# Kernel tuning notes

Hardware: AMD Instinct MI355X
Metric: run time of the kernel (lower is better)

## Reference

```python
import jax, jax.numpy as jnp
import numpy as np


def gru_cell(x, h, Wih, Whh, bih, bhh):
    # torch GRU cell, gate order r, z, n
    gi = x @ Wih.T + bih
    gh = h @ Whh.T + bhh
    ir, iz, inn = jnp.split(gi, 3, axis=-1)
    hr, hz, hn = jnp.split(gh, 3, axis=-1)
    r = jax.nn.sigmoid(ir + hr)
    z = jax.nn.sigmoid(iz + hz)
    n = jnp.tanh(inn + r * hn)
    return (1.0 - z) * n + z * h


def setup_inputs() -> dict:
    key = jax.random.key(0)
    ks = jax.random.split(key, 24)
    S, T, B, E, H, V = 64, 64, 32, 512, 1024, 32000
    sc_e = 1.0 / np.sqrt(E)
    sc_h = 1.0 / np.sqrt(H)

    def rn(i, shape, sc):
        return jax.random.normal(ks[i], shape, jnp.float32) * sc

    return {
        "src": jax.random.randint(ks[0], (S, B), 0, V),
        "trg": jax.random.randint(ks[1], (T, B), 0, V),
        "emb": rn(2, (V, E), 0.02),
        # encoder forward-direction GRU
        "Wih_f": rn(3, (3 * H, E), sc_e), "Whh_f": rn(4, (3 * H, H), sc_h),
        "bih_f": rn(5, (3 * H,), sc_h), "bhh_f": rn(6, (3 * H,), sc_h),
        # encoder backward-direction GRU
        "Wih_b": rn(7, (3 * H, E), sc_e), "Whh_b": rn(8, (3 * H, H), sc_h),
        "bih_b": rn(9, (3 * H,), sc_h), "bhh_b": rn(10, (3 * H,), sc_h),
        # attention: Linear(2H -> H) and scoring vector v
        "Wa": rn(11, (H, 2 * H), sc_h), "ba": rn(12, (H,), sc_h),
        "v": rn(13, (H,), sc_h),
        # decoder GRU: input is [embedded(E); context(H)]
        "Wih_d": rn(14, (3 * H, E + H), sc_h), "Whh_d": rn(15, (3 * H, H), sc_h),
        "bih_d": rn(16, (3 * H,), sc_h), "bhh_d": rn(17, (3 * H,), sc_h),
        # output head Linear(2H -> V)
        "Wout": rn(18, (V, 2 * H), sc_h), "bout": rn(19, (V,), sc_h),
    }


def reference(src, trg, emb, Wih_f, Whh_f, bih_f, bhh_f, Wih_b, Whh_b, bih_b, bhh_b,
              Wa, ba, v, Wih_d, Whh_d, bih_d, bhh_d, Wout, bout):
    S, B = src.shape
    H = Whh_f.shape[1]

    # ---- encoder: bidirectional GRU, fwd+bwd output halves summed ----
    src_emb = emb[src]  # [S, B, E]
    h0 = jnp.zeros((B, H), src_emb.dtype)

    def step_f(h, x):
        h2 = gru_cell(x, h, Wih_f, Whh_f, bih_f, bhh_f)
        return h2, h2

    def step_b(h, x):
        h2 = gru_cell(x, h, Wih_b, Whh_b, bih_b, bhh_b)
        return h2, h2

    h_fwd, out_f = jax.lax.scan(step_f, h0, src_emb)
    _, out_b_rev = jax.lax.scan(step_b, h0, src_emb[::-1])
    enc_out = out_f + out_b_rev[::-1]          # [S, B, H]
    enc_bt = enc_out.transpose(1, 0, 2)        # [B, S, H]

    # ---- decoder with teacher forcing (ratio fixed to 1.0) ----
    dec_tokens = jnp.concatenate([src[-1:], trg[:-1]], axis=0)  # [T, B]
    dec_emb = emb[dec_tokens]                                   # [T, B, E]

    def dec_step(h, e_t):
        # Bahdanau attention: relu(Linear([h; enc])) scored by v
        hrep = jnp.broadcast_to(h[:, None, :], enc_bt.shape)    # [B, S, H]
        energy = jax.nn.relu(jnp.concatenate([hrep, enc_bt], -1) @ Wa.T + ba)
        scores = energy @ v                                     # [B, S]
        a = jax.nn.softmax(scores, axis=1)
        ctx = jnp.einsum('bs,bsh->bh', a, enc_bt)               # [B, H]
        rnn_in = jnp.concatenate([e_t, ctx], axis=-1)           # [B, E+H]
        h_new = gru_cell(rnn_in, h, Wih_d, Whh_d, bih_d, bhh_d)
        logits = jnp.concatenate([h_new, ctx], -1) @ Wout.T + bout  # [B, V]
        return h_new, logits

    _, outputs = jax.lax.scan(dec_step, h_fwd, dec_emb)  # [T, B, V]
    return outputs
```

## Files before the change

kernel.cpp:

```cpp
#include <hip/hip_runtime.h>
#include <hip/hip_bf16.h>

#define S_ 64
#define T_ 64
#define B_ 32
#define E_ 512
#define H_ 1024
#define V_ 32000
#define H3 3072
#define H2 2048
#define EH 1536

typedef unsigned short u16;
typedef unsigned int u32;
typedef unsigned long long u64;
typedef __attribute__((ext_vector_type(8))) short bf16x8;
typedef __attribute__((ext_vector_type(4))) float f32x4;

#define MFMA3(ACC, AH_, AL_, BH_, BL_)                                              \
    ACC = __builtin_amdgcn_mfma_f32_16x16x32_bf16(AL_, BH_, ACC, 0, 0, 0);          \
    ACC = __builtin_amdgcn_mfma_f32_16x16x32_bf16(AH_, BL_, ACC, 0, 0, 0);          \
    ACC = __builtin_amdgcn_mfma_f32_16x16x32_bf16(AH_, BH_, ACC, 0, 0, 0);

__device__ __forceinline__ void splitf(float x, u16& h, u16& l) {
    u32 xb = __float_as_uint(x);
    u32 hb = (xb + 0x7FFFu + ((xb >> 16) & 1u)) & 0xFFFF0000u;
    h = (u16)(hb >> 16);
    float lf = x - __uint_as_float(hb);
    u32 lb = __float_as_uint(lf);
    l = (u16)((lb + 0x7FFFu + ((lb >> 16) & 1u)) >> 16);
}

__device__ __forceinline__ float bf2f(u16 v) { return __uint_as_float(((u32)v) << 16); }

__device__ __forceinline__ void load_lds16(const void* g, void* l) {
    __builtin_amdgcn_global_load_lds((const __attribute__((address_space(1))) u32*)g,
                                     (__attribute__((address_space(3))) u32*)l, 16, 0, 0);
}

__device__ __forceinline__ bf16x8 ld_sys16(const u16* p) {
    union { bf16x8 v; u64 q[2]; } u;
    const u64* q = (const u64*)p;
    u.q[0] = __hip_atomic_load(q,     __ATOMIC_RELAXED, __HIP_MEMORY_SCOPE_SYSTEM);
    u.q[1] = __hip_atomic_load(q + 1, __ATOMIC_RELAXED, __HIP_MEMORY_SCOPE_SYSTEM);
    return u.v;
}
__device__ __forceinline__ float ld_sysf(const float* p) {
    return __hip_atomic_load(p, __ATOMIC_RELAXED, __HIP_MEMORY_SCOPE_SYSTEM);
}
__device__ __forceinline__ void st_sysf(float* p, float v) {
    __hip_atomic_store(p, v, __ATOMIC_RELAXED, __HIP_MEMORY_SCOPE_SYSTEM);
}
__device__ __forceinline__ void st_sysu16(u16* p, u16 v) {
    __hip_atomic_store(p, v, __ATOMIC_RELAXED, __HIP_MEMORY_SCOPE_SYSTEM);
}

__device__ __forceinline__ void gbar(int* cnt, int* flag, int nblk, int blk, int& gen) {
    __syncthreads();
    if (threadIdx.x == 0) {
        gen += 1;
        asm volatile("s_waitcnt vmcnt(0)" ::: "memory");
        __hip_atomic_fetch_add(&cnt[(blk & 7) << 5], 1, __ATOMIC_RELAXED,
                               __HIP_MEMORY_SCOPE_SYSTEM);
        if (blk == 0) {
            const int target = nblk * gen;
            for (;;) {
                int sum = 0;
#pragma unroll
                for (int j = 0; j < 8; ++j)
                    sum += __hip_atomic_load(&cnt[j << 5], __ATOMIC_RELAXED,
                                             __HIP_MEMORY_SCOPE_SYSTEM);
                if (sum >= target) break;
                __builtin_amdgcn_s_sleep(2);
            }
#pragma unroll
            for (int j = 0; j < 8; ++j)
                __hip_atomic_store(&flag[j << 5], gen, __ATOMIC_RELAXED,
                                   __HIP_MEMORY_SCOPE_SYSTEM);
        } else {
            while (__hip_atomic_load(&flag[(blk & 7) << 5], __ATOMIC_RELAXED,
                                     __HIP_MEMORY_SCOPE_SYSTEM) < gen)
                __builtin_amdgcn_s_sleep(2);
        }
    }
    __syncthreads();
}

__global__ void k_embed_src_split(const int* __restrict__ src, const float* __restrict__ emb,
                                  u16* __restrict__ hi, u16* __restrict__ lo) {
    int row = blockIdx.x;
    int tok = src[row];
    int c = threadIdx.x * 4;
    float4 v = *reinterpret_cast<const float4*>(emb + (size_t)tok * E_ + c);
    ushort4 h, l;
    splitf(v.x, h.x, l.x); splitf(v.y, h.y, l.y);
    splitf(v.z, h.z, l.z); splitf(v.w, h.w, l.w);
    *reinterpret_cast<ushort4*>(hi + (size_t)row * E_ + c) = h;
    *reinterpret_cast<ushort4*>(lo + (size_t)row * E_ + c) = l;
}

__global__ void k_embed_dec_split(const int* __restrict__ src, const int* __restrict__ trg,
                                  const float* __restrict__ emb,
                                  u16* __restrict__ hi, u16* __restrict__ lo) {
    int row = blockIdx.x;
    int t = row >> 5, b = row & 31;
    int tok = (t == 0) ? src[(S_ - 1) * B_ + b] : trg[(t - 1) * B_ + b];
    int c = threadIdx.x * 4;
    float4 v = *reinterpret_cast<const float4*>(emb + (size_t)tok * E_ + c);
    ushort4 h, l;
    splitf(v.x, h.x, l.x); splitf(v.y, h.y, l.y);
    splitf(v.z, h.z, l.z); splitf(v.w, h.w, l.w);
    *reinterpret_cast<ushort4*>(hi + (size_t)row * E_ + c) = h;
    *reinterpret_cast<ushort4*>(lo + (size_t)row * E_ + c) = l;
}

__global__ __launch_bounds__(256) void k_split(const float* __restrict__ in, int ld, int cols4,
                                               u16* __restrict__ hi, u16* __restrict__ lo) {
    int c4 = blockIdx.x * 256 + threadIdx.x;
    if (c4 >= cols4) return;
    size_t r = blockIdx.y;
    float4 v = *reinterpret_cast<const float4*>(in + r * ld + (size_t)c4 * 4);
    ushort4 h, l;
    splitf(v.x, h.x, l.x); splitf(v.y, h.y, l.y);
    splitf(v.z, h.z, l.z); splitf(v.w, h.w, l.w);
    size_t o = (r * cols4 + c4) * 4;
    *reinterpret_cast<ushort4*>(hi + o) = h;
    *reinterpret_cast<ushort4*>(lo + o) = l;
}

__global__ __launch_bounds__(256) void k_split_sum_enc(
    const float* __restrict__ ef, const float* __restrict__ eb, float* __restrict__ es,
    u16* __restrict__ hi, u16* __restrict__ lo) {
    size_t r = blockIdx.y;
    int c4 = threadIdx.x * 4;
    float4 va = *reinterpret_cast<const float4*>(ef + r * H_ + c4);
    float4 vb = *reinterpret_cast<const float4*>(eb + r * H_ + c4);
    float4 v; v.x = va.x + vb.x; v.y = va.y + vb.y; v.z = va.z + vb.z; v.w = va.w + vb.w;
    *reinterpret_cast<float4*>(es + r * H_ + c4) = v;
    ushort4 h, l;
    splitf(v.x, h.x, l.x); splitf(v.y, h.y, l.y);
    splitf(v.z, h.z, l.z); splitf(v.w, h.w, l.w);
    *reinterpret_cast<ushort4*>(hi + r * H_ + c4) = h;
    *reinterpret_cast<ushort4*>(lo + r * H_ + c4) = l;
}

__global__ void k_wsplit_perm(const float* __restrict__ src, int ld, int coff,
                              u16* __restrict__ hi, u16* __restrict__ lo) {
    int r = blockIdx.x;
    int i = r / 3, g = r - i * 3;
    const float* p = src + (size_t)(g * H_ + i) * ld + coff;
    int c = threadIdx.x * 4;
    float4 v = *reinterpret_cast<const float4*>(p + c);
    ushort4 h, l;
    splitf(v.x, h.x, l.x); splitf(v.y, h.y, l.y);
    splitf(v.z, h.z, l.z); splitf(v.w, h.w, l.w);
    *reinterpret_cast<ushort4*>(hi + (size_t)r * H_ + c) = h;
    *reinterpret_cast<ushort4*>(lo + (size_t)r * H_ + c) = l;
}

__global__ __launch_bounds__(256, 2) void k_gemm_mfma3(
    const u16* __restrict__ Ah, const u16* __restrict__ Al,
    const u16* __restrict__ Bh, const u16* __restrict__ Bl,
    const float* __restrict__ bias, float* __restrict__ C,
    int ldc, int K)
{
    __shared__ u16 ls[4][128 * 32];
    const int tid = threadIdx.x;
    const int lane = tid & 63, w = tid >> 6;
    const int wr = w >> 1, wc = w & 1;
    const size_t m0 = (size_t)blockIdx.x * 128, n0 = (size_t)blockIdx.y * 128;

    const int c0 = (w * 2) * 64 + lane;
    const int r0 = c0 >> 2, kc0 = (c0 & 3) << 3;
    const size_t rstep = (size_t)16 * K;
    const u16* gAh = Ah + (m0 + r0) * K + kc0;
    const u16* gAl = Al + (m0 + r0) * K + kc0;
    const u16* gBh = Bh + (n0 + r0) * K + kc0;
    const u16* gBl = Bl + (n0 + r0) * K + kc0;
    const int lo0 = c0 * 8;

    const int frow = lane & 15, fk = (lane >> 4) << 3;
    const int offA = (wr * 64 + frow) * 32 + fk;
    const int offB = (wc * 64 + frow) * 32 + fk;

    f32x4 acc[4][4] = {};

    for (int k0 = 0; k0 < K; k0 += 32) {
        load_lds16(gAh + k0, &ls[0][lo0]);
        load_lds16(gAh + rstep + k0, &ls[0][lo0 + 512]);
        load_lds16(gAl + k0, &ls[1][lo0]);
        load_lds16(gAl + rstep + k0, &ls[1][lo0 + 512]);
        load_lds16(gBh + k0, &ls[2][lo0]);
        load_lds16(gBh + rstep + k0, &ls[2][lo0 + 512]);
        load_lds16(gBl + k0, &ls[3][lo0]);
        load_lds16(gBl + rstep + k0, &ls[3][lo0 + 512]);
        __syncthreads();

        bf16x8 fAh[4], fAl[4], fBh[4], fBl[4];
#pragma unroll
        for (int m = 0; m < 4; ++m) {
            fAh[m] = *reinterpret_cast<const bf16x8*>(&ls[0][offA + m * 512]);
            fAl[m] = *reinterpret_cast<const bf16x8*>(&ls[1][offA + m * 512]);
        }
#pragma unroll
        for (int n = 0; n < 4; ++n) {
            fBh[n] = *reinterpret_cast<const bf16x8*>(&ls[2][offB + n * 512]);
            fBl[n] = *reinterpret_cast<const bf16x8*>(&ls[3][offB + n * 512]);
        }
#pragma unroll
        for (int m = 0; m < 4; ++m)
#pragma unroll
            for (int n = 0; n < 4; ++n) {
                MFMA3(acc[m][n], fAh[m], fAl[m], fBh[n], fBl[n]);
            }
        __syncthreads();
    }

    const int crow0 = wr * 64 + ((lane >> 4) << 2);
    const int ccol0 = wc * 64 + (lane & 15);
#pragma unroll
    for (int n = 0; n < 4; ++n) {
        const size_t col = n0 + ccol0 + n * 16;
        const float bv = bias ? bias[col] : 0.f;
#pragma unroll
        for (int m = 0; m < 4; ++m)
#pragma unroll
            for (int r = 0; r < 4; ++r)
                C[(m0 + crow0 + m * 16 + r) * (size_t)ldc + col] = acc[m][n][r] + bv;
    }
}

__global__ __launch_bounds__(256) void k_enc_persist(
    const u16* __restrict__ whhf_h, const u16* __restrict__ whhf_l,
    const u16* __restrict__ whhb_h, const u16* __restrict__ whhb_l,
    const float* __restrict__ gi_f, const float* __restrict__ gi_b,
    const float* __restrict__ bhh_f, const float* __restrict__ bhh_b,
    u16* __restrict__ hfH0, u16* __restrict__ hfL0,
    u16* __restrict__ hfH1, u16* __restrict__ hfL1,
    u16* __restrict__ hbH0, u16* __restrict__ hbL0,
    u16* __restrict__ hbH1, u16* __restrict__ hbL1,
    float* __restrict__ enc_f, float* __restrict__ enc_b,
    int* __restrict__ cnt, int* __restrict__ flag)
{
    __shared__ __align__(16) char smem[107008];
    u16* lH = (u16*)smem;
    float* ex = (float*)(smem + 98304);
    float* hloc = (float*)(smem + 104704);

    const int blk = blockIdx.x, tid = threadIdx.x;
    const int lane = tid & 63, w = tid >> 6;
    const int dir = blk >> 6, c = blk & 63;
    const int i0 = c * 16;
    const size_t rowbase = (size_t)c * 48;
    const u16* WH = (dir ? whhb_h : whhf_h) + rowbase * 1024;
    const u16* WL = (dir ? whhb_l : whhf_l) + rowbase * 1024;
    const float* gi = dir ? gi_b : gi_f;
    const float* bhh = dir ? bhh_b : bhh_f;
    float* encd = dir ? enc_b : enc_f;
    int gen = 0;

    for (int ch = tid; ch < 6144; ch += 256) {
        int r = ch >> 7, kc = (ch & 127) << 3;
        *(bf16x8*)&lH[r * 1024 + (kc ^ ((r & 7) << 3))] =
            *(const bf16x8*)&WH[(size_t)r * 1024 + kc];
    }
    for (int q = tid; q < 512; q += 256) hloc[q] = 0.f;
    __syncthreads();

    const int frow = lane & 15, fk8 = (lane >> 4) << 3;
    const int cb = lane & 15, rb0 = (lane >> 4) << 2;

    for (int t = 0; t < 64; ++t) {
        const int a = t & 1;
        const u16* rH = dir ? (a ? hbH1 : hbH0) : (a ? hfH1 : hfH0);
        const u16* rL = dir ? (a ? hbL1 : hbL0) : (a ? hfL1 : hfL0);
        u16* oH = dir ? (a ? hbH0 : hbH1) : (a ? hfH0 : hfH1);
        u16* oL = dir ? (a ? hbL0 : hbL1) : (a ? hfL0 : hfL1);
        const int s = dir ? 63 - t : t;

        if (w < 2) {
            f32x4 acc0 = {}, acc1 = {};
            const int lrB = w * 16 + frow;
            const int bsw = (lrB & 7) << 3;
            const u16* gBl = WL + (size_t)lrB * 1024;
#pragma unroll 4
            for (int k0 = 0; k0 < 1024; k0 += 32) {
                int kc = k0 + fk8;
                bf16x8 bH = *(const bf16x8*)&lH[lrB * 1024 + (kc ^ bsw)];
                bf16x8 bL = *(const bf16x8*)&gBl[kc];
                bf16x8 aH0 = ld_sys16(&rH[frow * 1024 + kc]);
                bf16x8 aL0 = ld_sys16(&rL[frow * 1024 + kc]);
                bf16x8 aH1 = ld_sys16(&rH[(16 + frow) * 1024 + kc]);
                bf16x8 aL1 = ld_sys16(&rL[(16 + frow) * 1024 + kc]);
                MFMA3(acc0, aH0, aL0, bH, bL);
                MFMA3(acc1, aH1, aL1, bH, bL);
            }
            int pc = w * 16 + cb;
#pragma unroll
            for (int r = 0; r < 4; ++r) {
                ex[pc * 33 + rb0 + r] = acc0[r];
                ex[pc * 33 + 16 + rb0 + r] = acc1[r];
            }
        } else {
            f32x4 acc0 = {}, acc1 = {};
            const int m = w - 2;
            const int lrB = 32 + frow;
            const int bsw = (lrB & 7) << 3;
            const u16* gBl = WL + (size_t)lrB * 1024;
#pragma unroll 2
            for (int k0 = 0; k0 < 1024; k0 += 64) {
                {
                    int kc = k0 + fk8;
                    bf16x8 bH = *(const bf16x8*)&lH[lrB * 1024 + (kc ^ bsw)];
                    bf16x8 bL = *(const bf16x8*)&gBl[kc];
                    bf16x8 aH = ld_sys16(&rH[(m * 16 + frow) * 1024 + kc]);
                    bf16x8 aL = ld_sys16(&rL[(m * 16 + frow) * 1024 + kc]);
                    MFMA3(acc0, aH, aL, bH, bL);
                }
                {
                    int kc = k0 + 32 + fk8;
                    bf16x8 bH = *(const bf16x8*)&lH[lrB * 1024 + (kc ^ bsw)];
                    bf16x8 bL = *(const bf16x8*)&gBl[kc];
                    bf16x8 aH = ld_sys16(&rH[(m * 16 + frow) * 1024 + kc]);
                    bf16x8 aL = ld_sys16(&rL[(m * 16 + frow) * 1024 + kc]);
                    MFMA3(acc1, aH, aL, bH, bL);
                }
            }
            f32x4 accs = acc0 + acc1;
            int pc = 32 + cb;
#pragma unroll
            for (int r = 0; r < 4; ++r)
                ex[pc * 33 + m * 16 + rb0 + r] = accs[r];
        }
        __syncthreads();

        {
            const int il = tid & 15, bb = tid >> 4;
            const int i = i0 + il;
#pragma unroll
            for (int q = 0; q < 2; ++q) {
                int b = bb + q * 16;
                float ghr = ex[(3 * il + 0) * 33 + b] + bhh[i];
                float ghz = ex[(3 * il + 1) * 33 + b] + bhh[H_ + i];
                float ghn = ex[(3 * il + 2) * 33 + b] + bhh[2 * H_ + i];
                size_t gio = (size_t)(s * B_ + b) * H3 + i;
                float gir = gi[gio], giz = gi[gio + H_], gin = gi[gio + 2 * H_];
                float rr = 1.f / (1.f + expf(-(gir + ghr)));
                float zz = 1.f / (1.f + expf(-(giz + ghz)));
                float nn = tanhf(gin + rr * ghn);
                float hold = hloc[b * 16 + il];
                float hnew = (1.f - zz) * nn + zz * hold;
                hloc[b * 16 + il] = hnew;
                u16 hh, hl; splitf(hnew, hh, hl);
                st_sysu16(&oH[b * 1024 + i], hh);
                st_sysu16(&oL[b * 1024 + i], hl);
                encd[((size_t)b * 64 + s) * H_ + i] = hnew;
            }
        }
        gbar(cnt, flag, 128, blk, gen);
    }
}

__global__ __launch_bounds__(256) void k_dec_persist(
    const u16* __restrict__ wah, const u16* __restrict__ wal,
    const u16* __restrict__ wgh, const u16* __restrict__ wgl,
    const u16* __restrict__ wdh, const u16* __restrict__ wdl,
    const float* __restrict__ gi_e, const float* __restrict__ bhh_d,
    const float* __restrict__ ep, const float* __restrict__ vvec,
    const float* __restrict__ enc,
    u16* __restrict__ hH, u16* __restrict__ hL,
    float* __restrict__ hwa, float* __restrict__ scores,
    u16* __restrict__ ctxH, u16* __restrict__ ctxL,
    float* __restrict__ states, int* __restrict__ cnt, int* __restrict__ flag)
{
    __shared__ __align__(16) char smem[140288];
    u16* lWH  = (u16*)smem;
    u16* lWL  = (u16*)(smem + 32768);
    u16* lDH  = (u16*)(smem + 65536);
    float* lenc = (float*)(smem + 98304);
    float* ex1a = (float*)(smem + 131072);
    float* ex1b = (float*)(smem + 133120);
    float* ex2a = (float*)(smem + 135168);
    float* ex2b = (float*)(smem + 137216);
    float* aw   = (float*)(smem + 139264);
    float* hloc = (float*)(smem + 139520);

    const int bid = blockIdx.x, tid = threadIdx.x;
    const int lane = tid & 63, w = tid >> 6;
    const int frow = lane & 15, fk8 = (lane >> 4) << 3;
    const int b3 = bid >> 3, sl = bid & 7;
    int gen = 0;

    for (int ch = tid; ch < 2048; ch += 256) {
        int r = ch >> 7, kc = (ch & 127) << 3;
        int sw = kc ^ ((r & 7) << 3);
        const u16 *sH, *sL;
        if (r < 4) { sH = wah + ((size_t)bid * 4 + r) * 1024;
                     sL = wal + ((size_t)bid * 4 + r) * 1024; }
        else       { sH = wgh + ((size_t)bid * 12 + r - 4) * 1024;
                     sL = wgl + ((size_t)bid * 12 + r - 4) * 1024; }
        *(bf16x8*)&lWH[r * 1024 + sw] = *(const bf16x8*)&sH[kc];
        *(bf16x8*)&lWL[r * 1024 + sw] = *(const bf16x8*)&sL[kc];
    }
    for (int ch = tid; ch < 2048; ch += 256) {
        int r = ch >> 7, kc = (ch & 127) << 3;
        int sw = kc ^ ((r & 7) << 3);
        int rowg = (r < 12) ? bid * 12 + r : bid * 12;
        *(bf16x8*)&lDH[r * 1024 + sw] = *(const bf16x8*)&wdh[(size_t)rowg * 1024 + kc];
    }
    for (int ch = tid; ch < 2048; ch += 256) {
        int s = ch >> 5, c4 = (ch & 31) << 2;
        *(float4*)&lenc[s * 128 + c4] =
            *(const float4*)&enc[((size_t)b3 * 64 + s) * 1024 + sl * 128 + c4];
    }
    if (tid < 128) {
        int b = tid >> 2, u = bid * 4 + (tid & 3);
        hloc[tid] = bf2f(hH[b * 1024 + u]) + bf2f(hL[b * 1024 + u]);
    }
    float vreg[16];
#pragma unroll
    for (int i = 0; i < 16; ++i) vreg[i] = vvec[lane + i * 64];
    __syncthreads();

    const int mt = w & 1, kh = w >> 1;
    const int bsw = (frow & 7) << 3;
    const int rowg = (frow < 12) ? bid * 12 + frow : bid * 12;
    const u16* gDl = wdl + (size_t)rowg * 1024;
    const int exw = (mt * 16 + ((lane >> 4) << 2)) * 16 + frow;

    for (int t = 0; t < 64; ++t) {
        {
            float* exA = kh ? ex1b : ex1a;
            f32x4 acc = {};
            const int ar0 = (mt * 16 + frow) * 1024;
            const int ke = kh * 512 + 512;
#pragma unroll 4
            for (int k0 = kh * 512; k0 < ke; k0 += 32) {
                int kc = k0 + fk8;
                bf16x8 aH = ld_sys16(&hH[ar0 + kc]);
                bf16x8 aL = ld_sys16(&hL[ar0 + kc]);
                bf16x8 bH = *(const bf16x8*)&lWH[frow * 1024 + (kc ^ bsw)];
                bf16x8 bL = *(const bf16x8*)&lWL[frow * 1024 + (kc ^ bsw)];
                MFMA3(acc, aH, aL, bH, bL);
            }
#pragma unroll
            for (int r = 0; r < 4; ++r) exA[exw + r * 16] = acc[r];
        }
        __syncthreads();
        if (tid < 128) {
            int b = tid >> 2, col = tid & 3;
            st_sysf(&hwa[b * 1024 + bid * 4 + col],
                    ex1a[b * 16 + col] + ex1b[b * 16 + col]);
        }
        gbar(cnt, flag, 256, bid, gen);

#pragma unroll
        for (int q2 = 0; q2 < 2; ++q2) {
            int s = sl * 8 + w * 2 + q2;
            const float* epr = ep + ((size_t)b3 * 64 + s) * 1024;
            const float* hr = hwa + b3 * 1024;
            float a2 = 0.f;
#pragma unroll
            for (int i = 0; i < 16; ++i) {
                int j = lane + i * 64;
                a2 += fmaxf(ld_sysf(&hr[j]) + epr[j], 0.f) * vreg[i];
            }
            for (int off = 32; off; off >>= 1) a2 += __shfl_down(a2, off);
            if (lane == 0) st_sysf(&scores[b3 * 64 + s], a2);
        }
        gbar(cnt, flag, 256, bid, gen);

        if (tid < 64) {
            float sc = ld_sysf(&scores[b3 * 64 + tid]);
            float m = sc;
            for (int off = 32; off; off >>= 1) m = fmaxf(m, __shfl_xor(m, off));
            float e = expf(sc - m);
            float sum = e;
            for (int off = 32; off; off >>= 1) sum += __shfl_xor(sum, off);
            aw[tid] = e / sum;
        }
        __syncthreads();
        if (tid < 128) {
            int c = tid;
            float x = 0.f;
#pragma unroll 8
            for (int s = 0; s < 64; ++s) x += aw[s] * lenc[s * 128 + c];
            states[((size_t)t * 32 + b3) * 2048 + 1024 + sl * 128 + c] = x;
            u16 hh, hl; splitf(x, hh, hl);
            st_sysu16(&ctxH[b3 * 1024 + sl * 128 + c], hh);
            st_sysu16(&ctxL[b3 * 1024 + sl * 128 + c], hl);
        }
        gbar(cnt, flag, 256, bid, gen);

        {
            float* exD = kh ? ex2b : ex2a;
            f32x4 acc = {};
            const int ar0 = (mt * 16 + frow) * 1024;
            const int ke = kh * 512 + 512;
#pragma unroll 4
            for (int k0 = kh * 512; k0 < ke; k0 += 32) {
                int kc = k0 + fk8;
                bf16x8 aH = ld_sys16(&ctxH[ar0 + kc]);
                bf16x8 aL = ld_sys16(&ctxL[ar0 + kc]);
                bf16x8 bH = *(const bf16x8*)&lDH[frow * 1024 + (kc ^ bsw)];
                bf16x8 bL = *(const bf16x8*)&gDl[kc];
                MFMA3(acc, aH, aL, bH, bL);
            }
#pragma unroll
            for (int r = 0; r < 4; ++r) exD[exw + r * 16] = acc[r];
        }
        __syncthreads();
        if (tid < 128) {
            int b = tid >> 2, ui = tid & 3;
            int u = bid * 4 + ui;
            float gicr = ex2a[b * 16 + 3 * ui + 0] + ex2b[b * 16 + 3 * ui + 0];
            float gicz = ex2a[b * 16 + 3 * ui + 1] + ex2b[b * 16 + 3 * ui + 1];
            float gicn = ex2a[b * 16 + 3 * ui + 2] + ex2b[b * 16 + 3 * ui + 2];
            float ghr = ex1a[b * 16 + 4 + 3 * ui + 0] + ex1b[b * 16 + 4 + 3 * ui + 0] + bhh_d[u];
            float ghz = ex1a[b * 16 + 4 + 3 * ui + 1] + ex1b[b * 16 + 4 + 3 * ui + 1] + bhh_d[H_ + u];
            float ghn = ex1a[b * 16 + 4 + 3 * ui + 2] + ex1b[b * 16 + 4 + 3 * ui + 2] + bhh_d[2 * H_ + u];
            size_t ge = ((size_t)t * 32 + b) * 3072;
            float gir = gi_e[ge + u] + gicr;
            float giz = gi_e[ge + 1024 + u] + gicz;
            float gin = gi_e[ge + 2048 + u] + gicn;
            float rr = 1.f / (1.f + expf(-(gir + ghr)));
            float zz = 1.f / (1.f + expf(-(giz + ghz)));
            float nn = tanhf(gin + rr * ghn);
            float hold = hloc[tid];
            float hnew = (1.f - zz) * nn + zz * hold;
            hloc[tid] = hnew;
            u16 hh, hl; splitf(hnew, hh, hl);
            st_sysu16(&hH[b * 1024 + u], hh);
            st_sysu16(&hL[b * 1024 + u], hl);
            states[((size_t)t * 32 + b) * 2048 + u] = hnew;
        }
        gbar(cnt, flag, 256, bid, gen);
    }
}

extern "C" void kernel_launch(void* const* d_in, const int* in_sizes, int n_in,
                              void* d_out, int out_size, void* d_ws, size_t ws_size,
                              hipStream_t stream) {
    const int*   src   = (const int*)d_in[0];
    const int*   trg   = (const int*)d_in[1];
    const float* emb   = (const float*)d_in[2];
    const float* Wih_f = (const float*)d_in[3];
    const float* Whh_f = (const float*)d_in[4];
    const float* bih_f = (const float*)d_in[5];
    const float* bhh_f = (const float*)d_in[6];
    const float* Wih_b = (const float*)d_in[7];
    const float* Whh_b = (const float*)d_in[8];
    const float* bih_b = (const float*)d_in[9];
    const float* bhh_b = (const float*)d_in[10];
    const float* Wa    = (const float*)d_in[11];
    const float* ba    = (const float*)d_in[12];
    const float* vv    = (const float*)d_in[13];
    const float* Wih_d = (const float*)d_in[14];
    const float* Whh_d = (const float*)d_in[15];
    const float* bih_d = (const float*)d_in[16];
    const float* bhh_d = (const float*)d_in[17];
    const float* Wout  = (const float*)d_in[18];
    const float* bout  = (const float*)d_in[19];
    float* out = (float*)d_out;
    (void)in_sizes; (void)n_in; (void)out_size; (void)ws_size;

    float* w = (float*)d_ws;
    size_t o = 0;
    auto alloc = [&](size_t n) { float* p = w + o; o += n; return p; };
    float* gi_f  = alloc((size_t)S_ * B_ * H3);
    float* gi_b  = alloc((size_t)S_ * B_ * H3);
    float* enc_f = alloc((size_t)B_ * S_ * H_);
    float* enc_b = alloc((size_t)B_ * S_ * H_);
    float* enc   = alloc((size_t)B_ * S_ * H_);
    float* ep    = alloc((size_t)B_ * S_ * H_);
    float* hwa   = alloc((size_t)B_ * H_);
    float* scores = alloc(B_ * S_);
    float* barf  = alloc(1024);
    int* cntE  = (int*)barf;
    int* flagE = cntE + 256;
    int* cntD  = cntE + 512;
    int* flagD = cntE + 768;
    float* gi_e   = gi_f;
    float* states = gi_b;

    u16* wu = (u16*)(w + o);
    size_t ou = 0;
    auto alloc16 = [&](size_t n) { u16* p = wu + ou; ou += n; return p; };
    u16* semb_h  = alloc16((size_t)S_ * B_ * E_);  u16* semb_l  = alloc16((size_t)S_ * B_ * E_);
    u16* demb_h  = alloc16((size_t)T_ * B_ * E_);  u16* demb_l  = alloc16((size_t)T_ * B_ * E_);
    u16* wihf_h  = alloc16((size_t)H3 * E_);       u16* wihf_l  = alloc16((size_t)H3 * E_);
    u16* wihb_h  = alloc16((size_t)H3 * E_);       u16* wihb_l  = alloc16((size_t)H3 * E_);
    u16* wihd_h  = alloc16((size_t)H3 * E_);       u16* wihd_l  = alloc16((size_t)H3 * E_);
    u16* wae_h   = alloc16((size_t)H_ * H_);       u16* wae_l   = alloc16((size_t)H_ * H_);
    u16* enc_h   = alloc16((size_t)B_ * S_ * H_);  u16* enc_l   = alloc16((size_t)B_ * S_ * H_);
    u16* st_h    = alloc16((size_t)T_ * B_ * H2);  u16* st_l    = alloc16((size_t)T_ * B_ * H2);
    u16* wout_h  = alloc16((size_t)6400 * H2);     u16* wout_l  = alloc16((size_t)6400 * H2);
    u16* whhf_h  = alloc16((size_t)H3 * H_);       u16* whhf_l  = alloc16((size_t)H3 * H_);
    u16* whhb_h  = alloc16((size_t)H3 * H_);       u16* whhb_l  = alloc16((size_t)H3 * H_);
    u16* wgh     = alloc16((size_t)H3 * H_);       u16* wgl     = alloc16((size_t)H3 * H_);
    u16* wdh     = alloc16((size_t)H3 * H_);       u16* wdl     = alloc16((size_t)H3 * H_);
    u16* wah     = alloc16((size_t)H_ * H_);       u16* wal     = alloc16((size_t)H_ * H_);
    u16* hsf_h[2] = {alloc16(B_ * H_), alloc16(B_ * H_)};
    u16* hsf_l[2] = {alloc16(B_ * H_), alloc16(B_ * H_)};
    u16* hsb_h[2] = {alloc16(B_ * H_), alloc16(B_ * H_)};
    u16* hsb_l[2] = {alloc16(B_ * H_), alloc16(B_ * H_)};
    u16* ctx_h   = alloc16(B_ * H_);               u16* ctx_l   = alloc16(B_ * H_);

    hipMemsetAsync(barf, 0, 1024 * sizeof(float), stream);
    hipMemsetAsync(hsf_h[0], 0, B_ * H_ * sizeof(u16), stream);
    hipMemsetAsync(hsf_l[0], 0, B_ * H_ * sizeof(u16), stream);
    hipMemsetAsync(hsb_h[0], 0, B_ * H_ * sizeof(u16), stream);
    hipMemsetAsync(hsb_l[0], 0, B_ * H_ * sizeof(u16), stream);

    k_embed_src_split<<<S_ * B_, 128, 0, stream>>>(src, emb, semb_h, semb_l);
    k_embed_dec_split<<<T_ * B_, 128, 0, stream>>>(src, trg, emb, demb_h, demb_l);

    k_split<<<dim3(1, H3), 256, 0, stream>>>(Wih_f, E_, E_ / 4, wihf_h, wihf_l);
    k_split<<<dim3(1, H3), 256, 0, stream>>>(Wih_b, E_, E_ / 4, wihb_h, wihb_l);
    k_split<<<dim3(1, H3), 256, 0, stream>>>(Wih_d, EH, E_ / 4, wihd_h, wihd_l);
    k_split<<<dim3(1, H_), 256, 0, stream>>>(Wa + H_, H2, H_ / 4, wae_h, wae_l);
    k_split<<<dim3(1, H_), 256, 0, stream>>>(Wa, H2, H_ / 4, wah, wal);
    k_wsplit_perm<<<H3, 256, 0, stream>>>(Whh_f, H_, 0, whhf_h, whhf_l);
    k_wsplit_perm<<<H3, 256, 0, stream>>>(Whh_b, H_, 0, whhb_h, whhb_l);
    k_wsplit_perm<<<H3, 256, 0, stream>>>(Whh_d, H_, 0, wgh, wgl);
    k_wsplit_perm<<<H3, 256, 0, stream>>>(Wih_d, EH, E_, wdh, wdl);

    k_gemm_mfma3<<<dim3(16, 24), 256, 0, stream>>>(semb_h, semb_l, wihf_h, wihf_l,
                                                   bih_f, gi_f, H3, E_);
    k_gemm_mfma3<<<dim3(16, 24), 256, 0, stream>>>(semb_h, semb_l, wihb_h, wihb_l,
                                                   bih_b, gi_b, H3, E_);

    k_enc_persist<<<128, 256, 0, stream>>>(
        whhf_h, whhf_l, whhb_h, whhb_l, gi_f, gi_b, bhh_f, bhh_b,
        hsf_h[0], hsf_l[0], hsf_h[1], hsf_l[1],
        hsb_h[0], hsb_l[0], hsb_h[1], hsb_l[1],
        enc_f, enc_b, cntE, flagE);

    k_split_sum_enc<<<dim3(1, B_ * S_), 256, 0, stream>>>(enc_f, enc_b, enc, enc_h, enc_l);
    k_gemm_mfma3<<<dim3(16, 8), 256, 0, stream>>>(enc_h, enc_l, wae_h, wae_l,
                                                  ba, ep, H_, H_);
    k_gemm_mfma3<<<dim3(16, 24), 256, 0, stream>>>(demb_h, demb_l, wihd_h, wihd_l,
                                                   bih_d, gi_e, H3, E_);

    k_dec_persist<<<256, 256, 0, stream>>>(
        wah, wal, wgh, wgl, wdh, wdl, gi_e, bhh_d, ep, vv, enc,
        hsf_h[0], hsf_l[0], hwa, scores, ctx_h, ctx_l, states, cntD, flagD);

    k_split<<<dim3(2, T_ * B_), 256, 0, stream>>>(states, H2, H2 / 4, st_h, st_l);
    for (int p = 0; p < 5; ++p) {
        k_split<<<dim3(2, 6400), 256, 0, stream>>>(Wout + (size_t)p * 6400 * H2, H2,
                                                   H2 / 4, wout_h, wout_l);
        k_gemm_mfma3<<<dim3(16, 50), 256, 0, stream>>>(st_h, st_l, wout_h, wout_l,
                                                       bout + p * 6400,
                                                       out + (size_t)p * 6400, V_, H2);
    }
}
```

Measured before the change: 4.762 ms.

## Stage hidden state in LDS per step and split K across waves in encoder

The encoder persistent kernel no longer keeps the high half of its Whh slice resident in LDS. Each timestep it copies the shared hidden state (hi/lo bf16 halves) from global into swizzled LDS, so it is read from memory once per block instead of once per wave. The 2x3 output tiles are split along K into two halves, giving 12 balanced jobs (3 per wave), and the partial sums are reduced through two exchange buffers. Both weight halves are now streamed from global/L2 every step, and the larger LDS footprint plus an extra barrier per step add cost.

```diff
diff --git a/kernel.cpp b/kernel.cpp
--- a/kernel.cpp
+++ b/kernel.cpp
@@ -242,30 +242,25 @@
     float* __restrict__ enc_f, float* __restrict__ enc_b,
     int* __restrict__ cnt, int* __restrict__ flag)
 {
-    __shared__ __align__(16) char smem[107008];
-    u16* lH = (u16*)smem;
-    float* ex = (float*)(smem + 98304);
-    float* hloc = (float*)(smem + 104704);
+    __shared__ __align__(16) char smem[145792];
+    u16* lAh  = (u16*)smem;
+    u16* lAl  = (u16*)(smem + 65536);
+    float* ex0 = (float*)(smem + 131072);
+    float* ex1 = (float*)(smem + 137408);
+    float* hloc = (float*)(smem + 143744);
 
     const int blk = blockIdx.x, tid = threadIdx.x;
     const int lane = tid & 63, w = tid >> 6;
     const int dir = blk >> 6, c = blk & 63;
     const int i0 = c * 16;
-    const size_t rowbase = (size_t)c * 48;
-    const u16* WH = (dir ? whhb_h : whhf_h) + rowbase * 1024;
-    const u16* WL = (dir ? whhb_l : whhf_l) + rowbase * 1024;
+    const u16* WH = (dir ? whhb_h : whhf_h) + (size_t)c * 48 * 1024;
+    const u16* WL = (dir ? whhb_l : whhf_l) + (size_t)c * 48 * 1024;
     const float* gi = dir ? gi_b : gi_f;
     const float* bhh = dir ? bhh_b : bhh_f;
     float* encd = dir ? enc_b : enc_f;
     int gen = 0;
 
-    for (int ch = tid; ch < 6144; ch += 256) {
-        int r = ch >> 7, kc = (ch & 127) << 3;
-        *(bf16x8*)&lH[r * 1024 + (kc ^ ((r & 7) << 3))] =
-            *(const bf16x8*)&WH[(size_t)r * 1024 + kc];
-    }
     for (int q = tid; q < 512; q += 256) hloc[q] = 0.f;
-    __syncthreads();
 
     const int frow = lane & 15, fk8 = (lane >> 4) << 3;
     const int cb = lane & 15, rb0 = (lane >> 4) << 2;
@@ -278,59 +273,42 @@
         u16* oL = dir ? (a ? hbL0 : hbL1) : (a ? hfL0 : hfL1);
         const int s = dir ? 63 - t : t;
 
-        if (w < 2) {
-            f32x4 acc0 = {}, acc1 = {};
-            const int lrB = w * 16 + frow;
-            const int bsw = (lrB & 7) << 3;
-            const u16* gBl = WL + (size_t)lrB * 1024;
+#pragma unroll
+        for (int ch0 = 0; ch0 < 4096; ch0 += 256) {
+            int ch = ch0 + tid;
+            int r = ch >> 7, kc = (ch & 127) << 3;
+            int sw = kc ^ ((r & 7) << 3);
+            *(bf16x8*)&lAh[r * 1024 + sw] = ld_sys16(&rH[r * 1024 + kc]);
+            *(bf16x8*)&lAl[r * 1024 + sw] = ld_sys16(&rL[r * 1024 + kc]);
+        }
+        __syncthreads();
+
+#pragma unroll
+        for (int jj = 0; jj < 3; ++jj) {
+            const int j = w * 3 + jj;
+            const int m = j & 1;
+            const int n = (j >> 1) % 3;
+            const int kh = j / 6;
+            const int arow = m * 16 + frow;
+            const int asw = (arow & 7) << 3;
+            const u16* gBh = WH + (size_t)(n * 16 + frow) * 1024;
+            const u16* gBl = WL + (size_t)(n * 16 + frow) * 1024;
+            f32x4 acc = {};
+            const int ke = kh * 512 + 512;
 #pragma unroll 4
-            for (int k0 = 0; k0 < 1024; k0 += 32) {
+            for (int k0 = kh * 512; k0 < ke; k0 += 32) {
                 int kc = k0 + fk8;
-                bf16x8 bH = *(const bf16x8*)&lH[lrB * 1024 + (kc ^ bsw)];
+                bf16x8 aH = *(const bf16x8*)&lAh[arow * 1024 + (kc ^ asw)];
+                bf16x8 aL = *(const bf16x8*)&lAl[arow * 1024 + (kc ^ asw)];
+                bf16x8 bH = *(const bf16x8*)&gBh[kc];
                 bf16x8 bL = *(const bf16x8*)&gBl[kc];
-                bf16x8 aH0 = ld_sys16(&rH[frow * 1024 + kc]);
-                bf16x8 aL0 = ld_sys16(&rL[frow * 1024 + kc]);
-                bf16x8 aH1 = ld_sys16(&rH[(16 + frow) * 1024 + kc]);
-                bf16x8 aL1 = ld_sys16(&rL[(16 + frow) * 1024 + kc]);
-                MFMA3(acc0, aH0, aL0, bH, bL);
-                MFMA3(acc1, aH1, aL1, bH, bL);
+                MFMA3(acc, aH, aL, bH, bL);
             }
-            int pc = w * 16 + cb;
-#pragma unroll
-            for (int r = 0; r < 4; ++r) {
-                ex[pc * 33 + rb0 + r] = acc0[r];
-                ex[pc * 33 + 16 + rb0 + r] = acc1[r];
-            }
-        } else {
-            f32x4 acc0 = {}, acc1 = {};
-            const int m = w - 2;
-            const int lrB = 32 + frow;
-            const int bsw = (lrB & 7) << 3;
-            const u16* gBl = WL + (size_t)lrB * 1024;
-#pragma unroll 2
-            for (int k0 = 0; k0 < 1024; k0 += 64) {
-                {
-                    int kc = k0 + fk8;
-                    bf16x8 bH = *(const bf16x8*)&lH[lrB * 1024 + (kc ^ bsw)];
-                    bf16x8 bL = *(const bf16x8*)&gBl[kc];
-                    bf16x8 aH = ld_sys16(&rH[(m * 16 + frow) * 1024 + kc]);
-                    bf16x8 aL = ld_sys16(&rL[(m * 16 + frow) * 1024 + kc]);
-                    MFMA3(acc0, aH, aL, bH, bL);
-                }
-                {
-                    int kc = k0 + 32 + fk8;
-                    bf16x8 bH = *(const bf16x8*)&lH[lrB * 1024 + (kc ^ bsw)];
-                    bf16x8 bL = *(const bf16x8*)&gBl[kc];
-                    bf16x8 aH = ld_sys16(&rH[(m * 16 + frow) * 1024 + kc]);
-                    bf16x8 aL = ld_sys16(&rL[(m * 16 + frow) * 1024 + kc]);
-                    MFMA3(acc1, aH, aL, bH, bL);
-                }
-            }
-            f32x4 accs = acc0 + acc1;
-            int pc = 32 + cb;
+            float* exd = kh ? ex1 : ex0;
+            const int pc = n * 16 + cb;
 #pragma unroll
             for (int r = 0; r < 4; ++r)
-                ex[pc * 33 + m * 16 + rb0 + r] = accs[r];
+                exd[pc * 33 + m * 16 + rb0 + r] = acc[r];
         }
         __syncthreads();
 
@@ -340,9 +318,9 @@
 #pragma unroll
             for (int q = 0; q < 2; ++q) {
                 int b = bb + q * 16;
-                float ghr = ex[(3 * il + 0) * 33 + b] + bhh[i];
-                float ghz = ex[(3 * il + 1) * 33 + b] + bhh[H_ + i];
-                float ghn = ex[(3 * il + 2) * 33 + b] + bhh[2 * H_ + i];
+                float ghr = ex0[(3 * il + 0) * 33 + b] + ex1[(3 * il + 0) * 33 + b] + bhh[i];
+                float ghz = ex0[(3 * il + 1) * 33 + b] + ex1[(3 * il + 1) * 33 + b] + bhh[H_ + i];
+                float ghn = ex0[(3 * il + 2) * 33 + b] + ex1[(3 * il + 2) * 33 + b] + bhh[2 * H_ + i];
                 size_t gio = (size_t)(s * B_ + b) * H3 + i;
                 float gir = gi[gio], giz = gi[gio + H_], gin = gi[gio + 2 * H_];
                 float rr = 1.f / (1.f + expf(-(gir + ghr)));
```

Result: faster. 4.354 ms (-8.6%).
